# Optimization experiments

Measured on AMD Instinct MI355X. Metric: run time of the kernel, lower is better.

## Reference

```python
import jax, jax.numpy as jnp
import numpy as np

B, S, C, L, H = 128, 8, 120, 469, 64


def setup_inputs() -> dict:
    key = jax.random.key(0)
    kx, kk, kq, kv = jax.random.split(key, 4)
    scale = 1.0 / np.sqrt(L)
    x = jax.random.normal(kx, (B, S, C, L), dtype=jnp.float32)
    # nn.Linear(L, H, bias=False): y = x @ W^T with W:[H,L]; store as [L,H] so y = x @ W
    Wk = jax.random.normal(kk, (L, H), dtype=jnp.float32) * scale
    Wq = jax.random.normal(kq, (L, H), dtype=jnp.float32) * scale
    Wv = jax.random.normal(kv, (L, H), dtype=jnp.float32) * scale
    return {"x": x, "Wk": Wk, "Wq": Wq, "Wv": Wv}


def reference(x, Wk, Wq, Wv):
    b, s, c, l = x.shape
    h = Wk.shape[-1]
    # torch: x.view(S_, B, C_, L_) -- a raw reshape, not a permute
    xs = x.reshape(s, b, c, l)
    k = xs @ Wk  # (s, b, c, h)
    q = xs @ Wq
    v = xs @ Wv
    wei = jnp.einsum('sbch,sbdh->sbcd', q, k) * (h ** -0.5)
    wei = jax.nn.softmax(wei, axis=-1)  # dropout = identity in eval
    out = jnp.einsum('sbcd,sbdh->sbch', wei, v)  # (s, b, c, h)
    # torch: matrices.view(B, S_, C_, head_size) -- raw reshape again
    return out.reshape(b, s, c, h)
```

## Files before the change

### kernel.cpp

```cpp
#include <hip/hip_runtime.h>
#include <hip/hip_bf16.h>

typedef __attribute__((ext_vector_type(8))) short bf16x8;
typedef __attribute__((ext_vector_type(4))) float f32x4;
typedef float f32x4u __attribute__((ext_vector_type(4), aligned(4)));
typedef __attribute__((ext_vector_type(4))) short short4v;
typedef unsigned short ushort_t;

#define CC 120
#define LL 469
#define HH 64

constexpr int NBATCH = 1024;
constexpr int KSTEPS = 15;

constexpr int WB_SHORTS   = 8192;
constexpr int SMEM_BYTES  = 49152;
constexpr int WIMG_SHORTS = KSTEPS * WB_SHORTS;
constexpr int WIMG_BYTES  = WIMG_SHORTS * 2;

__device__ __forceinline__ ushort_t f2bf(float f) {
  __hip_bfloat16 h = __float2bfloat16(f);
  return __builtin_bit_cast(ushort_t, h);
}

__device__ __forceinline__ void gload_lds16(const void* g, void* l) {
  __builtin_amdgcn_global_load_lds(
      (const __attribute__((address_space(1))) unsigned int*)g,
      (__attribute__((address_space(3))) unsigned int*)l, 16, 0, 0);
}

__device__ __forceinline__ char* sptr(char* base, int row, int stride, int byteoff) {
  return base + row * stride + (byteoff ^ ((row & 7) << 4));
}

__global__ void prep_w(const float* __restrict__ Wk, const float* __restrict__ Wq,
                       const float* __restrict__ Wv, ushort_t* __restrict__ wimg) {
  int idx = blockIdx.x * 256 + threadIdx.x;
  int t = idx / WB_SHORTS;
  int r = idx % WB_SHORTS;
  int col = r / 40, kk = r % 40;
  float v = 0.f;
  if (r < 192 * 40 && kk < 32) {
    int kb = (t == 14) ? 437 : t * 32;
    int k = kb + kk;
    bool live = (k < LL) && (t < 14 || k >= 448);
    if (live) {
      int wsel = col >> 6, h = col & 63;
      const float* wp = (wsel == 0) ? Wk : (wsel == 1) ? Wq : Wv;
      v = wp[(size_t)k * HH + h];
    }
  }
  wimg[idx] = f2bf(v);
}

#define XISSUE(T, X0, X1, X2, X3)                                              \
  {                                                                            \
    const int _k = (((T) == 14) ? 437 : (T) * 32) + lg * 8;                    \
    X0 = *(const f32x4u*)(xr0 + _k);                                           \
    X1 = *(const f32x4u*)(xr0 + _k + 4);                                       \
    X2 = *(const f32x4u*)(xr1c + _k);                                          \
    X3 = *(const f32x4u*)(xr1c + _k + 4);                                      \
  }
#define WISSUE(T)                                                              \
  {                                                                            \
    const char* _src = (const char*)(wimg + (size_t)(T) * WB_SHORTS);          \
    char* _dst = (char*)(Wl + ((T) % 3) * WB_SHORTS);                          \
    _Pragma("unroll")                                                          \
    for (int _i = 0; _i < 4; ++_i) {                                           \
      int _c = wv + 4 * _i;                                                    \
      gload_lds16(_src + _c * 1024 + lane * 16, _dst + _c * 1024);             \
    }                                                                          \
  }
#define ENDREGION(N)                                                           \
  {                                                                            \
    __builtin_amdgcn_sched_barrier(0);                                         \
    asm volatile("s_waitcnt vmcnt(" #N ")" ::: "memory");                      \
    __builtin_amdgcn_sched_barrier(0);                                         \
    __builtin_amdgcn_s_barrier();                                              \
    __builtin_amdgcn_sched_barrier(0);                                         \
  }
#define COMPUTE(T, X0, X1, X2, X3)                                             \
  {                                                                            \
    const ushort_t* _wb = Wl + ((T) % 3) * WB_SHORTS;                          \
    bf16x8 _a0, _a1;                                                           \
    _Pragma("unroll")                                                          \
    for (int _j = 0; _j < 4; ++_j) {                                           \
      _a0[_j] = (short)f2bf(X0[_j]); _a0[4 + _j] = (short)f2bf(X1[_j]);        \
      _a1[_j] = (short)f2bf(X2[_j]); _a1[4 + _j] = (short)f2bf(X3[_j]);        \
    }                                                                          \
    _Pragma("unroll")                                                          \
    for (int _n = 0; _n < 12; ++_n) {                                          \
      bf16x8 _b = *(const bf16x8*)(_wb + (_n * 16 + lr) * 40 + lg * 8);        \
      acc[0][_n] = __builtin_amdgcn_mfma_f32_16x16x32_bf16(_a0, _b, acc[0][_n], 0, 0, 0); \
      acc[1][_n] = __builtin_amdgcn_mfma_f32_16x16x32_bf16(_a1, _b, acc[1][_n], 0, 0, 0); \
    }                                                                          \
  }

template <bool WIMG>
__global__ __launch_bounds__(256, 3)
void fused_regional_head(const float* __restrict__ x,
                         const float* __restrict__ Wk,
                         const float* __restrict__ Wq,
                         const float* __restrict__ Wv,
                         const ushort_t* __restrict__ wimg,
                         float* __restrict__ out) {
  __shared__ char smem[SMEM_BYTES];
  const int tid = threadIdx.x;
  const int lane = tid & 63;
  const int wv = tid >> 6;
  const int lr = lane & 15;
  const int lg = lane >> 4;
  const int batch = blockIdx.x;
  const size_t xbase = (size_t)batch * CC * LL;

  ushort_t* Wl = (ushort_t*)smem;

  const int row0 = wv * 32 + lr;
  const int row1 = wv * 32 + 16 + lr;
  const int row1c = (row1 < CC) ? row1 : (CC - 1);
  const float* xr0  = x + xbase + (size_t)row0 * LL;
  const float* xr1c = x + xbase + (size_t)row1c * LL;

  f32x4 acc[2][12];
#pragma unroll
  for (int m = 0; m < 2; ++m)
#pragma unroll
    for (int n = 0; n < 12; ++n) acc[m][n] = (f32x4){0.f, 0.f, 0.f, 0.f};

  if constexpr (WIMG) {
    f32x4u xA0, xA1, xA2, xA3, xB0, xB1, xB2, xB3;
    WISSUE(0);
    WISSUE(1);
    XISSUE(0, xA0, xA1, xA2, xA3);
    ENDREGION(0);
#pragma unroll
    for (int tt = 0; tt < 6; ++tt) {
      const int t = 2 * tt;
      WISSUE(t + 2);
      XISSUE(t + 1, xB0, xB1, xB2, xB3);
      COMPUTE(t, xA0, xA1, xA2, xA3);
      ENDREGION(8);
      WISSUE(t + 3);
      XISSUE(t + 2, xA0, xA1, xA2, xA3);
      COMPUTE(t + 1, xB0, xB1, xB2, xB3);
      ENDREGION(8);
    }
    WISSUE(14);
    XISSUE(13, xB0, xB1, xB2, xB3);
    COMPUTE(12, xA0, xA1, xA2, xA3);
    ENDREGION(8);
    XISSUE(14, xA0, xA1, xA2, xA3);
    COMPUTE(13, xB0, xB1, xB2, xB3);
    ENDREGION(0);
    COMPUTE(14, xA0, xA1, xA2, xA3);
  } else {
    for (int t = 0; t < KSTEPS; ++t) {
      const int kb = (t == 14) ? 437 : t * 32;
      f32x4u x0 = *(const f32x4u*)(xr0 + kb + lg * 8);
      f32x4u x1 = *(const f32x4u*)(xr0 + kb + lg * 8 + 4);
      f32x4u x2 = *(const f32x4u*)(xr1c + kb + lg * 8);
      f32x4u x3 = *(const f32x4u*)(xr1c + kb + lg * 8 + 4);
      bf16x8 a0, a1;
#pragma unroll
      for (int j = 0; j < 4; ++j) {
        a0[j] = (short)f2bf(x0[j]); a0[4 + j] = (short)f2bf(x1[j]);
        a1[j] = (short)f2bf(x2[j]); a1[4 + j] = (short)f2bf(x3[j]);
      }
#pragma unroll
      for (int n = 0; n < 12; ++n) {
        int col = n * 16 + lr;
        int wsel = col >> 6, h = col & 63;
        const float* wp = (wsel == 0) ? Wk : (wsel == 1) ? Wq : Wv;
        bf16x8 b;
#pragma unroll
        for (int j = 0; j < 8; ++j) {
          int k = kb + lg * 8 + j;
          bool live = (k < LL) && (t < 14 || k >= 448);
          b[j] = (short)f2bf(live ? wp[(size_t)k * HH + h] : 0.f);
        }
        acc[0][n] = __builtin_amdgcn_mfma_f32_16x16x32_bf16(a0, b, acc[0][n], 0, 0, 0);
        acc[1][n] = __builtin_amdgcn_mfma_f32_16x16x32_bf16(a1, b, acc[1][n], 0, 0, 0);
      }
    }
  }
  __syncthreads();

  char* Qb = smem;
  char* Kb = smem + 16384;
  char* Vb = smem + 32768;
  char* Pb = smem;
#pragma unroll
  for (int mt = 0; mt < 2; ++mt) {
#pragma unroll
    for (int r = 0; r < 4; ++r) {
      int row = wv * 32 + mt * 16 + lg * 4 + r;
#pragma unroll
      for (int n = 0; n < 4; ++n) {
        *(ushort_t*)sptr(Kb, row, 128, (n * 16 + lr) * 2) = f2bf(acc[mt][n][r]);
        *(ushort_t*)sptr(Qb, row, 128, (n * 16 + lr) * 2) = f2bf(acc[mt][4 + n][r]);
      }
    }
#pragma unroll
    for (int n = 0; n < 4; ++n) {
      short4v pk;
#pragma unroll
      for (int r = 0; r < 4; ++r) pk[r] = (short)f2bf(acc[mt][8 + n][r]);
      *(short4v*)sptr(Vb, n * 16 + lr, 256, (wv * 32 + mt * 16 + lg * 4) * 2) = pk;
    }
  }
  __syncthreads();

  f32x4 accw[2][8];
#pragma unroll
  for (int m = 0; m < 2; ++m)
#pragma unroll
    for (int n = 0; n < 8; ++n) accw[m][n] = (f32x4){0.f, 0.f, 0.f, 0.f};
#pragma unroll
  for (int ks = 0; ks < 2; ++ks) {
    bf16x8 a0 = *(const bf16x8*)sptr(Qb, wv * 32 + lr, 128, ks * 64 + lg * 16);
    bf16x8 a1 = *(const bf16x8*)sptr(Qb, wv * 32 + 16 + lr, 128, ks * 64 + lg * 16);
#pragma unroll
    for (int n = 0; n < 8; ++n) {
      bf16x8 b = *(const bf16x8*)sptr(Kb, n * 16 + lr, 128, ks * 64 + lg * 16);
      accw[0][n] = __builtin_amdgcn_mfma_f32_16x16x32_bf16(a0, b, accw[0][n], 0, 0, 0);
      accw[1][n] = __builtin_amdgcn_mfma_f32_16x16x32_bf16(a1, b, accw[1][n], 0, 0, 0);
    }
  }
  __syncthreads();

#pragma unroll
  for (int mt = 0; mt < 2; ++mt)
#pragma unroll
    for (int r = 0; r < 4; ++r) {
      float l[8];
      float m = -1e30f;
#pragma unroll
      for (int n = 0; n < 8; ++n) {
        float v = accw[mt][n][r] * 0.125f;
        if (n == 7 && lr >= 8) v = -1e30f;
        l[n] = v;
        m = fmaxf(m, v);
      }
#pragma unroll
      for (int off = 1; off < 16; off <<= 1) m = fmaxf(m, __shfl_xor(m, off));
      float s = 0.f;
#pragma unroll
      for (int n = 0; n < 8; ++n) {
        float p = __expf(l[n] - m);
        l[n] = p;
        s += p;
      }
#pragma unroll
      for (int off = 1; off < 16; off <<= 1) s += __shfl_xor(s, off);
      float inv = 1.f / s;
      int row = wv * 32 + mt * 16 + lg * 4 + r;
#pragma unroll
      for (int n = 0; n < 8; ++n)
        *(ushort_t*)sptr(Pb, row, 256, (n * 16 + lr) * 2) = f2bf(l[n] * inv);
    }

  f32x4 acco[2][4];
#pragma unroll
  for (int m = 0; m < 2; ++m)
#pragma unroll
    for (int n = 0; n < 4; ++n) acco[m][n] = (f32x4){0.f, 0.f, 0.f, 0.f};
#pragma unroll
  for (int ks = 0; ks < 4; ++ks) {
    bf16x8 a0 = *(const bf16x8*)sptr(Pb, wv * 32 + lr, 256, ks * 64 + lg * 16);
    bf16x8 a1 = *(const bf16x8*)sptr(Pb, wv * 32 + 16 + lr, 256, ks * 64 + lg * 16);
#pragma unroll
    for (int n = 0; n < 4; ++n) {
      bf16x8 b = *(const bf16x8*)sptr(Vb, n * 16 + lr, 256, ks * 64 + lg * 16);
      acco[0][n] = __builtin_amdgcn_mfma_f32_16x16x32_bf16(a0, b, acco[0][n], 0, 0, 0);
      acco[1][n] = __builtin_amdgcn_mfma_f32_16x16x32_bf16(a1, b, acco[1][n], 0, 0, 0);
    }
  }

  __syncthreads();
  float* Ob = (float*)smem;
#pragma unroll
  for (int mt = 0; mt < 2; ++mt)
#pragma unroll
    for (int r = 0; r < 4; ++r) {
      int row = wv * 32 + mt * 16 + lg * 4 + r;
      if (row < CC) {
#pragma unroll
        for (int n = 0; n < 4; ++n)
          Ob[row * 68 + n * 16 + lr] = acco[mt][n][r];
      }
    }
  __syncthreads();
  const size_t obase = (size_t)batch * CC * HH;
#pragma unroll
  for (int i = 0; i < 8; ++i) {
    int idx = i * 256 + tid;
    if (idx < 1920) {
      int row = idx >> 4;
      int c4 = (idx & 15) * 4;
      f32x4 v = *(const f32x4*)(Ob + row * 68 + c4);
      *(f32x4*)(out + obase + (size_t)idx * 4) = v;
    }
  }
}

extern "C" void kernel_launch(void* const* d_in, const int* in_sizes, int n_in,
                              void* d_out, int out_size, void* d_ws, size_t ws_size,
                              hipStream_t stream) {
  (void)in_sizes; (void)n_in; (void)out_size;
  const float* x  = (const float*)d_in[0];
  const float* Wk = (const float*)d_in[1];
  const float* Wq = (const float*)d_in[2];
  const float* Wv = (const float*)d_in[3];
  float* out = (float*)d_out;
  if (ws_size >= (size_t)WIMG_BYTES && d_ws != nullptr) {
    ushort_t* wimg = (ushort_t*)d_ws;
    prep_w<<<480, 256, 0, stream>>>(Wk, Wq, Wv, wimg);
    fused_regional_head<true><<<NBATCH, 256, 0, stream>>>(x, Wk, Wq, Wv, wimg, out);
  } else {
    fused_regional_head<false><<<NBATCH, 256, 0, stream>>>(x, Wk, Wq, Wv, nullptr, out);
  }
}
```

Baseline: 69.50 us.

## Load pre-swizzled weight fragments directly from global instead of staging through LDS

```diff
diff --git a/kernel.cpp b/kernel.cpp
--- a/kernel.cpp
+++ b/kernel.cpp
@@ -14,9 +14,8 @@
 constexpr int NBATCH = 1024;
 constexpr int KSTEPS = 15;
 
-constexpr int WB_SHORTS   = 8192;
 constexpr int SMEM_BYTES  = 49152;
-constexpr int WIMG_SHORTS = KSTEPS * WB_SHORTS;
+constexpr int WIMG_SHORTS = KSTEPS * 12 * 64 * 8;
 constexpr int WIMG_BYTES  = WIMG_SHORTS * 2;
 
 __device__ __forceinline__ ushort_t f2bf(float f) {
@@ -24,12 +23,6 @@
   return __builtin_bit_cast(ushort_t, h);
 }
 
-__device__ __forceinline__ void gload_lds16(const void* g, void* l) {
-  __builtin_amdgcn_global_load_lds(
-      (const __attribute__((address_space(1))) unsigned int*)g,
-      (__attribute__((address_space(3))) unsigned int*)l, 16, 0, 0);
-}
-
 __device__ __forceinline__ char* sptr(char* base, int row, int stride, int byteoff) {
   return base + row * stride + (byteoff ^ ((row & 7) << 4));
 }
@@ -37,19 +30,21 @@
 __global__ void prep_w(const float* __restrict__ Wk, const float* __restrict__ Wq,
                        const float* __restrict__ Wv, ushort_t* __restrict__ wimg) {
   int idx = blockIdx.x * 256 + threadIdx.x;
-  int t = idx / WB_SHORTS;
-  int r = idx % WB_SHORTS;
-  int col = r / 40, kk = r % 40;
+  int j = idx & 7;
+  int lane = (idx >> 3) & 63;
+  int tn = idx >> 9;
+  int n = tn % 12;
+  int t = tn / 12;
+  int lr = lane & 15, lg = lane >> 4;
+  int kb = (t == 14) ? 437 : t * 32;
+  int k = kb + lg * 8 + j;
+  int col = n * 16 + lr;
   float v = 0.f;
-  if (r < 192 * 40 && kk < 32) {
-    int kb = (t == 14) ? 437 : t * 32;
-    int k = kb + kk;
-    bool live = (k < LL) && (t < 14 || k >= 448);
-    if (live) {
-      int wsel = col >> 6, h = col & 63;
-      const float* wp = (wsel == 0) ? Wk : (wsel == 1) ? Wq : Wv;
-      v = wp[(size_t)k * HH + h];
-    }
+  bool live = (k < LL) && (t < 14 || k >= 448);
+  if (live) {
+    int wsel = col >> 6, h = col & 63;
+    const float* wp = (wsel == 0) ? Wk : (wsel == 1) ? Wq : Wv;
+    v = wp[(size_t)k * HH + h];
   }
   wimg[idx] = f2bf(v);
 }
@@ -62,43 +57,25 @@
     X2 = *(const f32x4u*)(xr1c + _k);                                          \
     X3 = *(const f32x4u*)(xr1c + _k + 4);                                      \
   }
-#define WISSUE(T)                                                              \
-  {                                                                            \
-    const char* _src = (const char*)(wimg + (size_t)(T) * WB_SHORTS);          \
-    char* _dst = (char*)(Wl + ((T) % 3) * WB_SHORTS);                          \
-    _Pragma("unroll")                                                          \
-    for (int _i = 0; _i < 4; ++_i) {                                           \
-      int _c = wv + 4 * _i;                                                    \
-      gload_lds16(_src + _c * 1024 + lane * 16, _dst + _c * 1024);             \
-    }                                                                          \
-  }
-#define ENDREGION(N)                                                           \
-  {                                                                            \
-    __builtin_amdgcn_sched_barrier(0);                                         \
-    asm volatile("s_waitcnt vmcnt(" #N ")" ::: "memory");                      \
-    __builtin_amdgcn_sched_barrier(0);                                         \
-    __builtin_amdgcn_s_barrier();                                              \
-    __builtin_amdgcn_sched_barrier(0);                                         \
-  }
 #define COMPUTE(T, X0, X1, X2, X3)                                             \
   {                                                                            \
-    const ushort_t* _wb = Wl + ((T) % 3) * WB_SHORTS;                          \
     bf16x8 _a0, _a1;                                                           \
     _Pragma("unroll")                                                          \
     for (int _j = 0; _j < 4; ++_j) {                                           \
       _a0[_j] = (short)f2bf(X0[_j]); _a0[4 + _j] = (short)f2bf(X1[_j]);        \
       _a1[_j] = (short)f2bf(X2[_j]); _a1[4 + _j] = (short)f2bf(X3[_j]);        \
     }                                                                          \
+    const ushort_t* _wt = wfrag + (size_t)(T) * 6144;                          \
     _Pragma("unroll")                                                          \
     for (int _n = 0; _n < 12; ++_n) {                                          \
-      bf16x8 _b = *(const bf16x8*)(_wb + (_n * 16 + lr) * 40 + lg * 8);        \
+      bf16x8 _b = *(const bf16x8*)(_wt + _n * 512);                            \
       acc[0][_n] = __builtin_amdgcn_mfma_f32_16x16x32_bf16(_a0, _b, acc[0][_n], 0, 0, 0); \
       acc[1][_n] = __builtin_amdgcn_mfma_f32_16x16x32_bf16(_a1, _b, acc[1][_n], 0, 0, 0); \
     }                                                                          \
   }
 
 template <bool WIMG>
-__global__ __launch_bounds__(256, 3)
+__global__ __launch_bounds__(256, 2)
 void fused_regional_head(const float* __restrict__ x,
                          const float* __restrict__ Wk,
                          const float* __restrict__ Wq,
@@ -114,13 +91,12 @@
   const int batch = blockIdx.x;
   const size_t xbase = (size_t)batch * CC * LL;
 
-  ushort_t* Wl = (ushort_t*)smem;
-
   const int row0 = wv * 32 + lr;
   const int row1 = wv * 32 + 16 + lr;
   const int row1c = (row1 < CC) ? row1 : (CC - 1);
   const float* xr0  = x + xbase + (size_t)row0 * LL;
   const float* xr1c = x + xbase + (size_t)row1c * LL;
+  const ushort_t* wfrag = wimg + (size_t)lane * 8;
 
   f32x4 acc[2][12];
 #pragma unroll
@@ -130,29 +106,15 @@
 
   if constexpr (WIMG) {
     f32x4u xA0, xA1, xA2, xA3, xB0, xB1, xB2, xB3;
-    WISSUE(0);
-    WISSUE(1);
     XISSUE(0, xA0, xA1, xA2, xA3);
-    ENDREGION(0);
-#pragma unroll
-    for (int tt = 0; tt < 6; ++tt) {
+#pragma unroll
+    for (int tt = 0; tt < 7; ++tt) {
       const int t = 2 * tt;
-      WISSUE(t + 2);
       XISSUE(t + 1, xB0, xB1, xB2, xB3);
       COMPUTE(t, xA0, xA1, xA2, xA3);
-      ENDREGION(8);
-      WISSUE(t + 3);
       XISSUE(t + 2, xA0, xA1, xA2, xA3);
       COMPUTE(t + 1, xB0, xB1, xB2, xB3);
-      ENDREGION(8);
-    }
-    WISSUE(14);
-    XISSUE(13, xB0, xB1, xB2, xB3);
-    COMPUTE(12, xA0, xA1, xA2, xA3);
-    ENDREGION(8);
-    XISSUE(14, xA0, xA1, xA2, xA3);
-    COMPUTE(13, xB0, xB1, xB2, xB3);
-    ENDREGION(0);
+    }
     COMPUTE(14, xA0, xA1, xA2, xA3);
   } else {
     for (int t = 0; t < KSTEPS; ++t) {
@@ -315,7 +277,7 @@
   float* out = (float*)d_out;
   if (ws_size >= (size_t)WIMG_BYTES && d_ws != nullptr) {
     ushort_t* wimg = (ushort_t*)d_ws;
-    prep_w<<<480, 256, 0, stream>>>(Wk, Wq, Wv, wimg);
+    prep_w<<<360, 256, 0, stream>>>(Wk, Wq, Wv, wimg);
     fused_regional_head<true><<<NBATCH, 256, 0, stream>>>(x, Wk, Wq, Wv, wimg, out);
   } else {
     fused_regional_head<false><<<NBATCH, 256, 0, stream>>>(x, Wk, Wq, Wv, nullptr, out);
```

Result: slower. 122.2 us (+75.9%).
